# Kernel tuning notes

Hardware: AMD Instinct MI355X
Metric: run time of the kernel (lower is better)

Reference implementation:

```python
import jax, jax.numpy as jnp
import numpy as np

N_NODES = 50000
N_EDGES = 800000
IN_CH = 128
HID = 128


def _linear_params(key, fan_in, fan_out):
    kw, kb = jax.random.split(key)
    bound = 1.0 / np.sqrt(fan_in)
    W = jax.random.uniform(kw, (fan_in, fan_out), jnp.float32, -bound, bound)
    b = jax.random.uniform(kb, (fan_out,), jnp.float32, -bound, bound)
    return W, b


def setup_inputs() -> dict:
    key = jax.random.key(0)
    ks = jax.random.split(key, 11)
    x = jax.random.normal(ks[0], (N_NODES, IN_CH), jnp.float32)
    guidance_features = jax.random.normal(ks[1], (N_NODES, HID), jnp.float32)
    edge_index = jax.random.randint(ks[2], (2, N_EDGES), 0, N_NODES, jnp.int64)
    node_W, node_b = _linear_params(ks[3], IN_CH, HID)
    nbr_W, nbr_b = _linear_params(ks[4], IN_CH, HID)
    gud_W, gud_b = _linear_params(ks[5], HID, HID)
    enc_W, enc_b = _linear_params(ks[6], 3 * HID, HID)
    vp_W1, vp_b1 = _linear_params(ks[7], HID, HID // 2)
    vp_W2, vp_b2 = _linear_params(ks[8], HID // 2, 1)
    pol_W1, pol_b1 = _linear_params(ks[9], HID, HID)
    pol_W2, pol_b2 = _linear_params(ks[10], HID, 1)
    return dict(x=x, edge_index=edge_index, guidance_features=guidance_features,
                node_W=node_W, node_b=node_b, nbr_W=nbr_W, nbr_b=nbr_b,
                gud_W=gud_W, gud_b=gud_b, enc_W=enc_W, enc_b=enc_b,
                vp_W1=vp_W1, vp_b1=vp_b1, vp_W2=vp_W2, vp_b2=vp_b2,
                pol_W1=pol_W1, pol_b1=pol_b1, pol_W2=pol_W2, pol_b2=pol_b2)


def reference(x, edge_index, guidance_features,
              node_W, node_b, nbr_W, nbr_b, gud_W, gud_b,
              enc_W, enc_b, vp_W1, vp_b1, vp_W2, vp_b2,
              pol_W1, pol_b1, pol_W2, pol_b2):
    row, col = edge_index[0], edge_index[1]
    # Edge-wise gathers feeding three linear transforms -> [E, 3*HID] state
    node_feat = x[row] @ node_W + node_b            # [E, HID]
    nbr_feat = x[col] @ nbr_W + nbr_b               # [E, HID]
    gud_feat = guidance_features[col] @ gud_W + gud_b  # [E, HID]
    state = jnp.concatenate([node_feat, nbr_feat, gud_feat], axis=1)
    # state_encoder (eval mode: dropout = identity)
    enc = jax.nn.relu(state @ enc_W + enc_b)        # [E, HID]
    # value_predictor
    value_preds = jax.nn.relu(enc @ vp_W1 + vp_b1) @ vp_W2 + vp_b2  # [E, 1]
    # policy_net
    action_probs = jax.nn.sigmoid(
        jax.nn.relu(enc @ pol_W1 + pol_b1) @ pol_W2 + pol_b2)      # [E, 1]
    actions = (action_probs > 0.5).astype(x.dtype)  # eval-mode actions
    value_loss = jnp.zeros((), x.dtype)             # eval mode, labels=None
    return value_preds, action_probs, actions, value_loss
```

## Files before the change

### kernel.cpp

```cpp
#include <hip/hip_runtime.h>
#include <math.h>

#define N_NODES 50000
#define N_EDGES 800000

typedef __attribute__((ext_vector_type(8))) short short8_t;
typedef __attribute__((ext_vector_type(4))) float float4_t;

union U8 { short8_t v; unsigned short u[8]; };

__device__ __forceinline__ unsigned short bf16_rn(float f) {
    unsigned u = __float_as_uint(f);
    u += 0x7fffu + ((u >> 16) & 1u);
    return (unsigned short)(u >> 16);
}
__device__ __forceinline__ float bf2f(unsigned short h) {
    return __uint_as_float((unsigned)h << 16);
}
__device__ __forceinline__ void split3(float f, unsigned short& s0,
                                       unsigned short& s1, unsigned short& s2) {
    s0 = bf16_rn(f);  float r = f - bf2f(s0);
    s1 = bf16_rn(r);  r -= bf2f(s1);
    s2 = bf16_rn(r);
}
__device__ __forceinline__ void split3t(float f, unsigned short& s0,
                                        unsigned short& s1, unsigned short& s2) {
    unsigned u = __float_as_uint(f);
    s0 = (unsigned short)(u >> 16);
    float r = f - bf2f(s0);
    unsigned v = __float_as_uint(r);
    s1 = (unsigned short)(v >> 16);
    float r2 = r - bf2f(s1);
    s2 = bf16_rn(r2);
}


__global__ __launch_bounds__(256) void prep_kernel(
    const float* __restrict__ node_W, const float* __restrict__ node_b,
    const float* __restrict__ nbr_W,  const float* __restrict__ nbr_b,
    const float* __restrict__ gud_W,  const float* __restrict__ gud_b,
    const float* __restrict__ enc_W,  const float* __restrict__ enc_b,
    const float* __restrict__ vp_W1,  const float* __restrict__ vp_b1,
    const float* __restrict__ vp_W2,  const float* __restrict__ pol_W1,
    const float* __restrict__ pol_b1, const float* __restrict__ pol_W2,
    unsigned short* __restrict__ BTn0, unsigned short* __restrict__ BTn1,
    unsigned short* __restrict__ BTn2,
    unsigned short* __restrict__ BTg0, unsigned short* __restrict__ BTg1,
    unsigned short* __restrict__ BTg2,
    unsigned short* __restrict__ BTw0, unsigned short* __restrict__ BTw1,
    unsigned short* __restrict__ BTw2,
    float* __restrict__ cb, float* __restrict__ b1c, float* __restrict__ W2c,
    int* __restrict__ flags)
{
    const int k = blockIdx.x;
    const int j = threadIdx.x;
    if (j < 128) {
        float a = 0.f, b = 0.f;
        #pragma unroll 4
        for (int m = 0; m < 128; ++m) {
            a = fmaf(node_W[k * 128 + m], enc_W[m * 128 + j], a);
            b = fmaf(gud_W [k * 128 + m], enc_W[(256 + m) * 128 + j], b);
        }
        size_t i1 = (size_t)j * 128 + k;
        split3(a, BTn0[i1], BTn1[i1], BTn2[i1]);
        split3(b, BTg0[i1], BTg1[i1], BTg2[i1]);
    } else {
        const int n = j - 128;
        float a = 0.f;
        #pragma unroll 4
        for (int m = 0; m < 128; ++m)
            a = fmaf(nbr_W[k * 128 + m], enc_W[(128 + m) * 128 + n], a);
        size_t i2 = (size_t)(128 + n) * 128 + k;
        split3(a, BTn0[i2], BTn1[i2], BTn2[i2]);
    }
    if (j < 192) {
        float wv = (j < 64) ? vp_W1[k * 64 + j] : pol_W1[k * 128 + (j - 64)];
        size_t iw = (size_t)j * 128 + k;
        split3(wv, BTw0[iw], BTw1[iw], BTw2[iw]);
    }
    if (k == 0) {
        if (j < 128) {
            float cc = enc_b[j];
            for (int m = 0; m < 128; ++m) {
                cc = fmaf(node_b[m], enc_W[m * 128 + j], cc);
                cc = fmaf(nbr_b [m], enc_W[(128 + m) * 128 + j], cc);
                cc = fmaf(gud_b [m], enc_W[(256 + m) * 128 + j], cc);
            }
            cb[j] = cc;
        }
        if (j < 192) {
            b1c[j] = (j < 64) ? vp_b1[j] : pol_b1[j - 64];
            W2c[j] = (j < 64) ? vp_W2[j] : pol_W2[j - 64];
        }
        if (j < 64) {
            const int l = j, li = l & 15, lq = l >> 4;
            U8 A, B;
            #pragma unroll
            for (int u = 0; u < 8; ++u) { A.u[u] = 0; B.u[u] = 0; }
            if (lq == 0) {
                A.u[0] = bf16_rn((float)(li + 1));
                A.u[1] = bf16_rn(1.0f);
                B.u[0] = bf16_rn(1.0f);
                B.u[1] = bf16_rn((float)(100 * (li + 1)));
            }
            float4_t d = (float4_t){0.f, 0.f, 0.f, 0.f};
            d = __builtin_amdgcn_mfma_f32_16x16x32_bf16(A.v, B.v, d, 0, 0, 0);
            if (l == 17) {
                flags[0] = (fabsf(d[2] - 702.f) < 1.0f) ? 1 : 0;
            }
        }
    }
}

__global__ __launch_bounds__(256, 3) void node_kernel(
    const float* __restrict__ x, const float* __restrict__ g,
    const unsigned short* __restrict__ BTn0, const unsigned short* __restrict__ BTn1,
    const unsigned short* __restrict__ BTn2,
    const unsigned short* __restrict__ BTg0, const unsigned short* __restrict__ BTg1,
    const unsigned short* __restrict__ BTg2,
    const float* __restrict__ cb, const int* __restrict__ flags,
    float* __restrict__ P, float* __restrict__ Q)
{
    __shared__ unsigned short a0s[4 * 64 * 8];
    __shared__ unsigned short a1s[4 * 64 * 8];
    __shared__ unsigned short a2s[4 * 64 * 8];
    const int t = threadIdx.x;
    const int w = t >> 6, lane = t & 63;
    const int i16 = lane & 15, q = lane >> 4;
    const int base = blockIdx.x * 64;
    const int swap = flags[0];
    const int el = t >> 2, hh = t & 3;
    int nodeL = base + el; if (nodeL > N_NODES - 1) nodeL = N_NODES - 1;
    const float* xrow = x + (size_t)nodeL * 128 + hh * 8;
    const float* grow = g + (size_t)nodeL * 128 + hh * 8;

    float4_t acc[4][4];
    #pragma unroll
    for (int mt = 0; mt < 4; ++mt)
        #pragma unroll
        for (int nt = 0; nt < 4; ++nt) acc[mt][nt] = (float4_t){0.f, 0.f, 0.f, 0.f};

    float4 pv0 = *(const float4*)(xrow);
    float4 pv1 = *(const float4*)(xrow + 4);

    for (int kc = 0; kc < 8; ++kc) {
        U8 s0, s1, s2;
        {
            float e[8] = {pv0.x, pv0.y, pv0.z, pv0.w, pv1.x, pv1.y, pv1.z, pv1.w};
            #pragma unroll
            for (int u = 0; u < 8; ++u) split3t(e[u], s0.u[u], s1.u[u], s2.u[u]);
        }
        __syncthreads();
        {
            size_t off = ((size_t)hh * 64 + el) * 8;
            *(short8_t*)(a0s + off) = s0.v;
            *(short8_t*)(a1s + off) = s1.v;
            *(short8_t*)(a2s + off) = s2.v;
        }
        __syncthreads();
        if (kc < 7) {
            const float* nsrc = (kc + 1 < 4) ? (xrow + (kc + 1) * 32)
                                             : (grow + (kc + 1 - 4) * 32);
            pv0 = *(const float4*)(nsrc);
            pv1 = *(const float4*)(nsrc + 4);
        }
        if (kc < 4) {
            short8_t b0[4], b1v[4], b2v[4];
            #pragma unroll
            for (int ntl = 0; ntl < 4; ++ntl) {
                int ntg = w + ntl * 4;
                size_t roff = ((size_t)(ntg * 16 + i16)) * 128 + kc * 32 + q * 8;
                b0[ntl]  = *(const short8_t*)(BTn0 + roff);
                b1v[ntl] = *(const short8_t*)(BTn1 + roff);
                b2v[ntl] = *(const short8_t*)(BTn2 + roff);
            }
            #pragma unroll
            for (int mt = 0; mt < 4; ++mt) {
                size_t aoff = ((size_t)q * 64 + mt * 16 + i16) * 8;
                short8_t a0 = *(const short8_t*)(a0s + aoff);
                short8_t a1 = *(const short8_t*)(a1s + aoff);
                short8_t a2 = *(const short8_t*)(a2s + aoff);
                #pragma unroll
                for (int ntl = 0; ntl < 4; ++ntl) {
                    float4_t c = acc[mt][ntl];
                    c = __builtin_amdgcn_mfma_f32_16x16x32_bf16(a0, b0[ntl],  c, 0, 0, 0);
                    c = __builtin_amdgcn_mfma_f32_16x16x32_bf16(a0, b1v[ntl], c, 0, 0, 0);
                    c = __builtin_amdgcn_mfma_f32_16x16x32_bf16(a1, b0[ntl],  c, 0, 0, 0);
                    c = __builtin_amdgcn_mfma_f32_16x16x32_bf16(a0, b2v[ntl], c, 0, 0, 0);
                    c = __builtin_amdgcn_mfma_f32_16x16x32_bf16(a1, b1v[ntl], c, 0, 0, 0);
                    c = __builtin_amdgcn_mfma_f32_16x16x32_bf16(a2, b0[ntl],  c, 0, 0, 0);
                    acc[mt][ntl] = c;
                }
            }
        } else {
            short8_t b0[2], b1v[2], b2v[2];
            #pragma unroll
            for (int ntl = 0; ntl < 2; ++ntl) {
                int ntg = w + (ntl + 2) * 4;
                size_t roff = ((size_t)((ntg - 8) * 16 + i16)) * 128 + (kc - 4) * 32 + q * 8;
                b0[ntl]  = *(const short8_t*)(BTg0 + roff);
                b1v[ntl] = *(const short8_t*)(BTg1 + roff);
                b2v[ntl] = *(const short8_t*)(BTg2 + roff);
            }
            #pragma unroll
            for (int mt = 0; mt < 4; ++mt) {
                size_t aoff = ((size_t)q * 64 + mt * 16 + i16) * 8;
                short8_t a0 = *(const short8_t*)(a0s + aoff);
                short8_t a1 = *(const short8_t*)(a1s + aoff);
                short8_t a2 = *(const short8_t*)(a2s + aoff);
                #pragma unroll
                for (int ntl = 0; ntl < 2; ++ntl) {
                    float4_t c = acc[mt][ntl + 2];
                    c = __builtin_amdgcn_mfma_f32_16x16x32_bf16(a0, b0[ntl],  c, 0, 0, 0);
                    c = __builtin_amdgcn_mfma_f32_16x16x32_bf16(a0, b1v[ntl], c, 0, 0, 0);
                    c = __builtin_amdgcn_mfma_f32_16x16x32_bf16(a1, b0[ntl],  c, 0, 0, 0);
                    c = __builtin_amdgcn_mfma_f32_16x16x32_bf16(a0, b2v[ntl], c, 0, 0, 0);
                    c = __builtin_amdgcn_mfma_f32_16x16x32_bf16(a1, b1v[ntl], c, 0, 0, 0);
                    c = __builtin_amdgcn_mfma_f32_16x16x32_bf16(a2, b0[ntl],  c, 0, 0, 0);
                    acc[mt][ntl + 2] = c;
                }
            }
        }
    }

    if (!swap) {
        #pragma unroll
        for (int mt = 0; mt < 4; ++mt)
            #pragma unroll
            for (int ntl = 0; ntl < 4; ++ntl) {
                int ntg = w + ntl * 4;
                int chan = ntg * 16 + i16;
                bool isP = (ntg < 8);
                float bias = isP ? cb[chan] : 0.f;
                #pragma unroll
                for (int r = 0; r < 4; ++r) {
                    int node = base + mt * 16 + q * 4 + r;
                    if (node < N_NODES) {
                        if (isP) P[(size_t)node * 128 + chan] = acc[mt][ntl][r] + bias;
                        else     Q[(size_t)node * 128 + (chan - 128)] = acc[mt][ntl][r];
                    }
                }
            }
    } else {
        #pragma unroll
        for (int mt = 0; mt < 4; ++mt) {
            int node = base + mt * 16 + i16;
            if (node < N_NODES) {
                #pragma unroll
                for (int ntl = 0; ntl < 4; ++ntl) {
                    int ntg = w + ntl * 4;
                    int chanb = ntg * 16 + q * 4;
                    bool isP = (ntg < 8);
                    float4 vv;
                    vv.x = acc[mt][ntl][0] + (isP ? cb[chanb + 0] : 0.f);
                    vv.y = acc[mt][ntl][1] + (isP ? cb[chanb + 1] : 0.f);
                    vv.z = acc[mt][ntl][2] + (isP ? cb[chanb + 2] : 0.f);
                    vv.w = acc[mt][ntl][3] + (isP ? cb[chanb + 3] : 0.f);
                    if (isP) *(float4*)(P + (size_t)node * 128 + chanb) = vv;
                    else     *(float4*)(Q + (size_t)node * 128 + chanb - 128) = vv;
                }
            }
        }
    }
}

#define STAGE(BUF)                                                              \
    {                                                                           \
        U8 g0[2], g1[2], g2[2];                                                 \
        _Pragma("unroll")                                                       \
        for (int i = 0; i < 4; ++i) {                                           \
            float ev[4] = {fmaxf(pv[i].x + qv[i].x, 0.f),                       \
                           fmaxf(pv[i].y + qv[i].y, 0.f),                       \
                           fmaxf(pv[i].z + qv[i].z, 0.f),                       \
                           fmaxf(pv[i].w + qv[i].w, 0.f)};                      \
            _Pragma("unroll")                                                   \
            for (int u = 0; u < 4; ++u) {                                       \
                int idx = i * 4 + u;                                            \
                split3t(ev[u], g0[idx >> 3].u[idx & 7], g1[idx >> 3].u[idx & 7],\
                        g2[idx >> 3].u[idx & 7]);                               \
            }                                                                   \
        }                                                                       \
        _Pragma("unroll")                                                       \
        for (int hb = 0; hb < 2; ++hb) {                                        \
            size_t off = ((size_t)(2 * hh + hb) * 128 + el) * 8;                \
            *(short8_t*)(enc0[BUF] + off) = g0[hb].v;                           \
            *(short8_t*)(enc1[BUF] + off) = g1[hb].v;                           \
            *(short8_t*)(enc2[BUF] + off) = g2[hb].v;                           \
        }                                                                       \
    }

#define LOADB(KC, D0, D1, D2)                                                   \
    {                                                                           \
        _Pragma("unroll")                                                       \
        for (int ntl = 0; ntl < 3; ++ntl) {                                     \
            size_t roff = ((size_t)((ntg0 + ntl) * 16 + i16)) * 128             \
                          + (KC) * 32 + q * 8;                                  \
            D0[ntl] = *(const short8_t*)(BTw0 + roff);                          \
            D1[ntl] = *(const short8_t*)(BTw1 + roff);                          \
            D2[ntl] = *(const short8_t*)(BTw2 + roff);                          \
        }                                                                       \
    }

#define PREFETCH_PQ(KC)                                                         \
    {                                                                           \
        _Pragma("unroll")                                                       \
        for (int i = 0; i < 4; ++i) {                                           \
            pv[i] = *(const float4*)(Pp + ((KC) + 1) * 32 + i * 4);             \
            qv[i] = *(const float4*)(Qp + ((KC) + 1) * 32 + i * 4);             \
        }                                                                       \
    }

#define MFMA_PHASE(BUF, B0, B1, B2)                                             \
    {                                                                           \
        _Pragma("unroll")                                                       \
        for (int mt = 0; mt < 8; ++mt) {                                        \
            size_t aoff = ((size_t)q * 128 + mt * 16 + i16) * 8;                \
            short8_t a0 = *(const short8_t*)(enc0[BUF] + aoff);                 \
            short8_t a1 = *(const short8_t*)(enc1[BUF] + aoff);                 \
            short8_t a2 = *(const short8_t*)(enc2[BUF] + aoff);                 \
            _Pragma("unroll")                                                   \
            for (int ntl = 0; ntl < 3; ++ntl) {                                 \
                float4_t c = acc[mt][ntl];                                      \
                c = __builtin_amdgcn_mfma_f32_16x16x32_bf16(a0, B0[ntl], c, 0, 0, 0); \
                c = __builtin_amdgcn_mfma_f32_16x16x32_bf16(a0, B1[ntl], c, 0, 0, 0); \
                c = __builtin_amdgcn_mfma_f32_16x16x32_bf16(a1, B0[ntl], c, 0, 0, 0); \
                c = __builtin_amdgcn_mfma_f32_16x16x32_bf16(a0, B2[ntl], c, 0, 0, 0); \
                c = __builtin_amdgcn_mfma_f32_16x16x32_bf16(a1, B1[ntl], c, 0, 0, 0); \
                c = __builtin_amdgcn_mfma_f32_16x16x32_bf16(a2, B0[ntl], c, 0, 0, 0); \
                acc[mt][ntl] = c;                                               \
            }                                                                   \
        }                                                                       \
    }

__global__ __launch_bounds__(256, 2) void edge_kernel(
    const int* __restrict__ ei,
    const float* __restrict__ P, const float* __restrict__ Q,
    const unsigned short* __restrict__ BTw0, const unsigned short* __restrict__ BTw1,
    const unsigned short* __restrict__ BTw2,
    const float* __restrict__ b1c, const float* __restrict__ W2c,
    const float* __restrict__ vp_b2, const float* __restrict__ pol_b2,
    const int* __restrict__ flags,
    float* __restrict__ out)
{
    __shared__ unsigned short enc0[2][4 * 128 * 8];
    __shared__ unsigned short enc1[2][4 * 128 * 8];
    __shared__ unsigned short enc2[2][4 * 128 * 8];
    __shared__ float vpart[512], ppart[512];

    const int t = threadIdx.x;
    const int w = t >> 6, lane = t & 63;
    const int i16 = lane & 15, q = lane >> 4;
    const int e0 = blockIdx.x * 128;
    const int ntg0 = w * 3;
    const int el = t >> 1, hh = t & 1;
    const int swap = flags[0];

    const int rowI = ei[e0 + el];
    const int colI = ei[N_EDGES + e0 + el];
    const float* Pp = P + (size_t)rowI * 128 + hh * 16;
    const float* Qp = Q + (size_t)colI * 128 + hh * 16;

    float4_t acc[8][3];
    #pragma unroll
    for (int mt = 0; mt < 8; ++mt)
        #pragma unroll
        for (int nt = 0; nt < 3; ++nt) acc[mt][nt] = (float4_t){0.f, 0.f, 0.f, 0.f};

    float4 pv[4], qv[4];
    #pragma unroll
    for (int i = 0; i < 4; ++i) {
        pv[i] = *(const float4*)(Pp + i * 4);
        qv[i] = *(const float4*)(Qp + i * 4);
    }
    short8_t bA0[3], bA1[3], bA2[3], bB0[3], bB1[3], bB2[3];
    LOADB(0, bA0, bA1, bA2);

    STAGE(0);
    __syncthreads();
    PREFETCH_PQ(0);
    LOADB(1, bB0, bB1, bB2);
    MFMA_PHASE(0, bA0, bA1, bA2);
    STAGE(1);
    __syncthreads();
    PREFETCH_PQ(1);
    LOADB(2, bA0, bA1, bA2);
    MFMA_PHASE(1, bB0, bB1, bB2);
    STAGE(0);
    __syncthreads();
    PREFETCH_PQ(2);
    LOADB(3, bB0, bB1, bB2);
    MFMA_PHASE(0, bA0, bA1, bA2);
    STAGE(1);
    __syncthreads();
    MFMA_PHASE(1, bB0, bB1, bB2);

    if (!swap) {
        #pragma unroll
        for (int mt = 0; mt < 8; ++mt) {
            float vs[4] = {0.f, 0.f, 0.f, 0.f}, ps[4] = {0.f, 0.f, 0.f, 0.f};
            #pragma unroll
            for (int ntl = 0; ntl < 3; ++ntl) {
                int ntg = ntg0 + ntl;
                int n = ntg * 16 + i16;
                float b1s = b1c[n], w2s = W2c[n];
                bool isv = (ntg < 4);
                #pragma unroll
                for (int r = 0; r < 4; ++r) {
                    float hv = fmaxf(acc[mt][ntl][r] + b1s, 0.f) * w2s;
                    if (isv) vs[r] += hv; else ps[r] += hv;
                }
            }
            #pragma unroll
            for (int off = 1; off < 16; off <<= 1)
                #pragma unroll
                for (int r = 0; r < 4; ++r) {
                    vs[r] += __shfl_xor(vs[r], off, 64);
                    ps[r] += __shfl_xor(ps[r], off, 64);
                }
            if (i16 == 0)
                #pragma unroll
                for (int r = 0; r < 4; ++r) {
                    int eidx = mt * 16 + q * 4 + r;
                    vpart[w * 128 + eidx] = vs[r];
                    ppart[w * 128 + eidx] = ps[r];
                }
        }
    } else {
        #pragma unroll
        for (int mt = 0; mt < 8; ++mt) {
            float v = 0.f, p = 0.f;
            #pragma unroll
            for (int ntl = 0; ntl < 3; ++ntl) {
                int ntg = ntg0 + ntl;
                bool isv = (ntg < 4);
                #pragma unroll
                for (int r = 0; r < 4; ++r) {
                    int n = ntg * 16 + q * 4 + r;
                    float hv = fmaxf(acc[mt][ntl][r] + b1c[n], 0.f) * W2c[n];
                    if (isv) v += hv; else p += hv;
                }
            }
            v += __shfl_xor(v, 16, 64); v += __shfl_xor(v, 32, 64);
            p += __shfl_xor(p, 16, 64); p += __shfl_xor(p, 32, 64);
            if (q == 0) {
                int eidx = mt * 16 + i16;
                vpart[w * 128 + eidx] = v;
                ppart[w * 128 + eidx] = p;
            }
        }
    }
    __syncthreads();
    if (t < 128) {
        float v  = vpart[t] + vpart[128 + t] + vpart[256 + t] + vpart[384 + t] + vp_b2[0];
        float pl = ppart[t] + ppart[128 + t] + ppart[256 + t] + ppart[384 + t] + pol_b2[0];
        float prob = 1.0f / (1.0f + expf(-pl));
        int e = e0 + t;
        out[e] = v;
        out[N_EDGES + e] = prob;
        out[2 * N_EDGES + e] = (prob > 0.5f) ? 1.0f : 0.0f;
    }
    if (blockIdx.x == 0 && t == 0) out[3 * N_EDGES] = 0.0f;
}

extern "C" void kernel_launch(void* const* d_in, const int* in_sizes, int n_in,
                              void* d_out, int out_size, void* d_ws, size_t ws_size,
                              hipStream_t stream) {
    const float* x      = (const float*)d_in[0];
    const int*   ei     = (const int*)  d_in[1];
    const float* gf     = (const float*)d_in[2];
    const float* node_W = (const float*)d_in[3];
    const float* node_b = (const float*)d_in[4];
    const float* nbr_W  = (const float*)d_in[5];
    const float* nbr_b  = (const float*)d_in[6];
    const float* gud_W  = (const float*)d_in[7];
    const float* gud_b  = (const float*)d_in[8];
    const float* enc_W  = (const float*)d_in[9];
    const float* enc_b  = (const float*)d_in[10];
    const float* vp_W1  = (const float*)d_in[11];
    const float* vp_b1  = (const float*)d_in[12];
    const float* vp_W2  = (const float*)d_in[13];
    const float* vp_b2  = (const float*)d_in[14];
    const float* pol_W1 = (const float*)d_in[15];
    const float* pol_b1 = (const float*)d_in[16];
    const float* pol_W2 = (const float*)d_in[17];
    const float* pol_b2 = (const float*)d_in[18];
    float* out = (float*)d_out;

    unsigned char* wsb = (unsigned char*)d_ws;
    unsigned short* BTn0 = (unsigned short*)(wsb + 0);
    unsigned short* BTn1 = (unsigned short*)(wsb + 65536);
    unsigned short* BTn2 = (unsigned short*)(wsb + 131072);
    unsigned short* BTg0 = (unsigned short*)(wsb + 196608);
    unsigned short* BTg1 = (unsigned short*)(wsb + 229376);
    unsigned short* BTg2 = (unsigned short*)(wsb + 262144);
    unsigned short* BTw0 = (unsigned short*)(wsb + 294912);
    unsigned short* BTw1 = (unsigned short*)(wsb + 344064);
    unsigned short* BTw2 = (unsigned short*)(wsb + 393216);
    float* cb   = (float*)(wsb + 442368);
    float* b1c  = (float*)(wsb + 442880);
    float* W2c  = (float*)(wsb + 443648);
    int*   flags= (int*)  (wsb + 444416);
    float* Pd   = (float*)(wsb + 444480);
    float* Qd   = Pd + (size_t)N_NODES * 128;

    prep_kernel<<<dim3(128), dim3(256), 0, stream>>>(
        node_W, node_b, nbr_W, nbr_b, gud_W, gud_b, enc_W, enc_b,
        vp_W1, vp_b1, vp_W2, pol_W1, pol_b1, pol_W2,
        BTn0, BTn1, BTn2, BTg0, BTg1, BTg2, BTw0, BTw1, BTw2,
        cb, b1c, W2c, flags);

    node_kernel<<<dim3((N_NODES + 63) / 64), dim3(256), 0, stream>>>(
        x, gf, BTn0, BTn1, BTn2, BTg0, BTg1, BTg2, cb, flags, Pd, Qd);

    edge_kernel<<<dim3(N_EDGES / 128), dim3(256), 0, stream>>>(
        ei, Pd, Qd, BTw0, BTw1, BTw2, b1c, W2c, vp_b2, pol_b2, flags, out);
}
```

Measured before the change: 543.7 us.

## Drop third bf16 split of edge activations and restructure edge kernel staging

The edge kernel now splits the ReLU'd P+Q activations into two bf16 pieces instead of three. That removes one LDS buffer and one of the six MFMAs per k-step (a2*B0). The software pipeline, which double-buffered and prefetched B and P/Q loads, is replaced by two stage-then-compute rounds that each cover two k-chunks. LDS moves to dynamic allocation and launch bounds rise to 3 blocks per SU to raise occupancy. The catch is some accuracy loss from the dropped low-order term and less overlap between global loads and MFMA work.

Result: faster. 508.7 us (-6.4%).

```diff
diff --git a/kernel.cpp b/kernel.cpp
--- a/kernel.cpp
+++ b/kernel.cpp
@@ -32,6 +32,13 @@
     s1 = (unsigned short)(v >> 16);
     float r2 = r - bf2f(s1);
     s2 = bf16_rn(r2);
+}
+__device__ __forceinline__ void split2t(float f, unsigned short& s0,
+                                        unsigned short& s1) {
+    unsigned u = __float_as_uint(f);
+    s0 = (unsigned short)(u >> 16);
+    float r = f - bf2f(s0);
+    s1 = bf16_rn(r);
 }
 
 
@@ -264,9 +271,15 @@
     }
 }
 
-#define STAGE(BUF)                                                              \
+#define STAGE_KC(KC, KCL)                                                       \
     {                                                                           \
-        U8 g0[2], g1[2], g2[2];                                                 \
+        float4 pv[4], qv[4];                                                    \
+        _Pragma("unroll")                                                       \
+        for (int i = 0; i < 4; ++i) {                                           \
+            pv[i] = *(const float4*)(Pp + (KC) * 32 + i * 4);                   \
+            qv[i] = *(const float4*)(Qp + (KC) * 32 + i * 4);                   \
+        }                                                                       \
+        U8 g0[2], g1[2];                                                        \
         _Pragma("unroll")                                                       \
         for (int i = 0; i < 4; ++i) {                                           \
             float ev[4] = {fmaxf(pv[i].x + qv[i].x, 0.f),                       \
@@ -276,63 +289,47 @@
             _Pragma("unroll")                                                   \
             for (int u = 0; u < 4; ++u) {                                       \
                 int idx = i * 4 + u;                                            \
-                split3t(ev[u], g0[idx >> 3].u[idx & 7], g1[idx >> 3].u[idx & 7],\
-                        g2[idx >> 3].u[idx & 7]);                               \
+                split2t(ev[u], g0[idx >> 3].u[idx & 7], g1[idx >> 3].u[idx & 7]);\
             }                                                                   \
         }                                                                       \
         _Pragma("unroll")                                                       \
         for (int hb = 0; hb < 2; ++hb) {                                        \
-            size_t off = ((size_t)(2 * hh + hb) * 128 + el) * 8;                \
-            *(short8_t*)(enc0[BUF] + off) = g0[hb].v;                           \
-            *(short8_t*)(enc1[BUF] + off) = g1[hb].v;                           \
-            *(short8_t*)(enc2[BUF] + off) = g2[hb].v;                           \
+            size_t off = ((size_t)((KCL) * 4 + 2 * hh + hb) * 128 + el) * 8;    \
+            *(short8_t*)(enc0 + off) = g0[hb].v;                                \
+            *(short8_t*)(enc1 + off) = g1[hb].v;                                \
         }                                                                       \
     }
 
-#define LOADB(KC, D0, D1, D2)                                                   \
+#define MFMA_KC(KC, KCL)                                                        \
     {                                                                           \
+        short8_t b0[3], b1f[3], b2f[3];                                         \
         _Pragma("unroll")                                                       \
         for (int ntl = 0; ntl < 3; ++ntl) {                                     \
             size_t roff = ((size_t)((ntg0 + ntl) * 16 + i16)) * 128             \
                           + (KC) * 32 + q * 8;                                  \
-            D0[ntl] = *(const short8_t*)(BTw0 + roff);                          \
-            D1[ntl] = *(const short8_t*)(BTw1 + roff);                          \
-            D2[ntl] = *(const short8_t*)(BTw2 + roff);                          \
+            b0[ntl]  = *(const short8_t*)(BTw0 + roff);                         \
+            b1f[ntl] = *(const short8_t*)(BTw1 + roff);                         \
+            b2f[ntl] = *(const short8_t*)(BTw2 + roff);                         \
         }                                                                       \
-    }
-
-#define PREFETCH_PQ(KC)                                                         \
-    {                                                                           \
-        _Pragma("unroll")                                                       \
-        for (int i = 0; i < 4; ++i) {                                           \
-            pv[i] = *(const float4*)(Pp + ((KC) + 1) * 32 + i * 4);             \
-            qv[i] = *(const float4*)(Qp + ((KC) + 1) * 32 + i * 4);             \
-        }                                                                       \
-    }
-
-#define MFMA_PHASE(BUF, B0, B1, B2)                                             \
-    {                                                                           \
         _Pragma("unroll")                                                       \
         for (int mt = 0; mt < 8; ++mt) {                                        \
-            size_t aoff = ((size_t)q * 128 + mt * 16 + i16) * 8;                \
-            short8_t a0 = *(const short8_t*)(enc0[BUF] + aoff);                 \
-            short8_t a1 = *(const short8_t*)(enc1[BUF] + aoff);                 \
-            short8_t a2 = *(const short8_t*)(enc2[BUF] + aoff);                 \
+            size_t aoff = ((size_t)((KCL) * 4 + q) * 128 + mt * 16 + i16) * 8;  \
+            short8_t a0 = *(const short8_t*)(enc0 + aoff);                      \
+            short8_t a1 = *(const short8_t*)(enc1 + aoff);                      \
             _Pragma("unroll")                                                   \
             for (int ntl = 0; ntl < 3; ++ntl) {                                 \
                 float4_t c = acc[mt][ntl];                                      \
-                c = __builtin_amdgcn_mfma_f32_16x16x32_bf16(a0, B0[ntl], c, 0, 0, 0); \
-                c = __builtin_amdgcn_mfma_f32_16x16x32_bf16(a0, B1[ntl], c, 0, 0, 0); \
-                c = __builtin_amdgcn_mfma_f32_16x16x32_bf16(a1, B0[ntl], c, 0, 0, 0); \
-                c = __builtin_amdgcn_mfma_f32_16x16x32_bf16(a0, B2[ntl], c, 0, 0, 0); \
-                c = __builtin_amdgcn_mfma_f32_16x16x32_bf16(a1, B1[ntl], c, 0, 0, 0); \
-                c = __builtin_amdgcn_mfma_f32_16x16x32_bf16(a2, B0[ntl], c, 0, 0, 0); \
+                c = __builtin_amdgcn_mfma_f32_16x16x32_bf16(a0, b0[ntl],  c, 0, 0, 0); \
+                c = __builtin_amdgcn_mfma_f32_16x16x32_bf16(a0, b1f[ntl], c, 0, 0, 0); \
+                c = __builtin_amdgcn_mfma_f32_16x16x32_bf16(a1, b0[ntl],  c, 0, 0, 0); \
+                c = __builtin_amdgcn_mfma_f32_16x16x32_bf16(a0, b2f[ntl], c, 0, 0, 0); \
+                c = __builtin_amdgcn_mfma_f32_16x16x32_bf16(a1, b1f[ntl], c, 0, 0, 0); \
                 acc[mt][ntl] = c;                                               \
             }                                                                   \
         }                                                                       \
     }
 
-__global__ __launch_bounds__(256, 2) void edge_kernel(
+__global__ __launch_bounds__(256, 3) void edge_kernel(
     const int* __restrict__ ei,
     const float* __restrict__ P, const float* __restrict__ Q,
     const unsigned short* __restrict__ BTw0, const unsigned short* __restrict__ BTw1,
@@ -342,10 +339,11 @@
     const int* __restrict__ flags,
     float* __restrict__ out)
 {
-    __shared__ unsigned short enc0[2][4 * 128 * 8];
-    __shared__ unsigned short enc1[2][4 * 128 * 8];
-    __shared__ unsigned short enc2[2][4 * 128 * 8];
-    __shared__ float vpart[512], ppart[512];
+    extern __shared__ unsigned short dynlds[];
+    unsigned short* enc0 = dynlds;
+    unsigned short* enc1 = dynlds + 8 * 128 * 8;
+    float* vpart = (float*)(dynlds + 16 * 128 * 8);
+    float* ppart = vpart + 512;
 
     const int t = threadIdx.x;
     const int w = t >> 6, lane = t & 63;
@@ -360,39 +358,26 @@
     const float* Pp = P + (size_t)rowI * 128 + hh * 16;
     const float* Qp = Q + (size_t)colI * 128 + hh * 16;
 
+    STAGE_KC(0, 0);
+    STAGE_KC(1, 1);
+    __syncthreads();
+
     float4_t acc[8][3];
     #pragma unroll
     for (int mt = 0; mt < 8; ++mt)
         #pragma unroll
         for (int nt = 0; nt < 3; ++nt) acc[mt][nt] = (float4_t){0.f, 0.f, 0.f, 0.f};
 
-    float4 pv[4], qv[4];
-    #pragma unroll
-    for (int i = 0; i < 4; ++i) {
-        pv[i] = *(const float4*)(Pp + i * 4);
-        qv[i] = *(const float4*)(Qp + i * 4);
-    }
-    short8_t bA0[3], bA1[3], bA2[3], bB0[3], bB1[3], bB2[3];
-    LOADB(0, bA0, bA1, bA2);
-
-    STAGE(0);
+    MFMA_KC(0, 0);
+    MFMA_KC(1, 1);
     __syncthreads();
-    PREFETCH_PQ(0);
-    LOADB(1, bB0, bB1, bB2);
-    MFMA_PHASE(0, bA0, bA1, bA2);
-    STAGE(1);
+
+    STAGE_KC(2, 0);
+    STAGE_KC(3, 1);
     __syncthreads();
-    PREFETCH_PQ(1);
-    LOADB(2, bA0, bA1, bA2);
-    MFMA_PHASE(1, bB0, bB1, bB2);
-    STAGE(0);
-    __syncthreads();
-    PREFETCH_PQ(2);
-    LOADB(3, bB0, bB1, bB2);
-    MFMA_PHASE(0, bA0, bA1, bA2);
-    STAGE(1);
-    __syncthreads();
-    MFMA_PHASE(1, bB0, bB1, bB2);
+
+    MFMA_KC(2, 0);
+    MFMA_KC(3, 1);
 
     if (!swap) {
         #pragma unroll
@@ -503,6 +488,14 @@
     float* Pd   = (float*)(wsb + 444480);
     float* Qd   = Pd + (size_t)N_NODES * 128;
 
+    static int attr_set = 0;
+    if (!attr_set) {
+        (void)hipFuncSetAttribute((const void*)edge_kernel,
+                                  hipFuncAttributeMaxDynamicSharedMemorySize,
+                                  36864);
+        attr_set = 1;
+    }
+
     prep_kernel<<<dim3(128), dim3(256), 0, stream>>>(
         node_W, node_b, nbr_W, nbr_b, gud_W, gud_b, enc_W, enc_b,
         vp_W1, vp_b1, vp_W2, pol_W1, pol_b1, pol_W2,
@@ -512,6 +505,6 @@
     node_kernel<<<dim3((N_NODES + 63) / 64), dim3(256), 0, stream>>>(
         x, gf, BTn0, BTn1, BTn2, BTg0, BTg1, BTg2, cb, flags, Pd, Qd);
 
-    edge_kernel<<<dim3(N_EDGES / 128), dim3(256), 0, stream>>>(
+    edge_kernel<<<dim3(N_EDGES / 128), dim3(256), 36864, stream>>>(
         ei, Pd, Qd, BTw0, BTw1, BTw2, b1c, W2c, vp_b2, pol_b2, flags, out);
 }
```
